# Performance work log

Measured on AMD Instinct MI355X. Metric: run time of the kernel, lower is better.

Reference implementation:

```python
import jax, jax.numpy as jnp
import numpy as np
import math

NUM_HEADS = 16
HIDDEN = 1024
MLP = 4096
SEQ = 2048
HEAD_DIM = HIDDEN // NUM_HEADS  # 64
EPS = 1e-5


def setup_inputs() -> dict:
    key = jax.random.key(0)
    ks = jax.random.split(key, 16)
    s = 0.02
    inp = {
        "x": jax.random.normal(ks[0], (SEQ, HIDDEN), jnp.float32),
        "rope_cos": jnp.cos(jnp.arange(SEQ, dtype=jnp.float32)[:, None] * (1.0 / (10000.0 ** (jnp.arange(HEAD_DIM // 2, dtype=jnp.float32) * 2 / HEAD_DIM)))[None, :]),
        "rope_sin": jnp.sin(jnp.arange(SEQ, dtype=jnp.float32)[:, None] * (1.0 / (10000.0 ** (jnp.arange(HEAD_DIM // 2, dtype=jnp.float32) * 2 / HEAD_DIM)))[None, :]),
        "norm0_w": jnp.ones((HIDDEN,), jnp.float32),
        "norm0_b": jnp.zeros((HIDDEN,), jnp.float32),
        "norm1_w": jnp.ones((HIDDEN,), jnp.float32),
        "norm1_b": jnp.zeros((HIDDEN,), jnp.float32),
        "wqkv_w": jax.random.normal(ks[1], (3 * HIDDEN, HIDDEN), jnp.float32) * s,
        "wqkv_b": jnp.zeros((3 * HIDDEN,), jnp.float32),
        "wo_w": jax.random.normal(ks[2], (HIDDEN, HIDDEN), jnp.float32) * s,
        "wo_b": jnp.zeros((HIDDEN,), jnp.float32),
        "up_w": jax.random.normal(ks[3], (MLP, HIDDEN), jnp.float32) * s,
        "up_b": jnp.zeros((MLP,), jnp.float32),
        "down_w": jax.random.normal(ks[4], (HIDDEN, MLP), jnp.float32) * s,
        "down_b": jnp.zeros((HIDDEN,), jnp.float32),
        # 4 packed sequences of length 512 each
        "input_row_offsets": jnp.array([0, 512, 1024, 1536, 2048], jnp.int32),
    }
    return inp


def _layernorm(x, w, b):
    m = jnp.mean(x, axis=-1, keepdims=True)
    v = jnp.mean((x - m) ** 2, axis=-1, keepdims=True)
    return (x - m) * jax.lax.rsqrt(v + EPS) * w + b


def _rope(t, cos, sin):
    # t: [S, nh, hd]; cos/sin: [S, hd/2] -> complex rotation of adjacent pairs
    S, nh, hd = t.shape
    t2 = t.reshape(S, nh, hd // 2, 2)
    re, im = t2[..., 0], t2[..., 1]
    c = cos[:, None, :]
    s = sin[:, None, :]
    out = jnp.stack([re * c - im * s, re * s + im * c], axis=-1)
    return out.reshape(S, nh, hd)


def _block(x, rope_cos, rope_sin, norm0_w, norm0_b, wqkv_w, wqkv_b, wo_w, wo_b,
           up_w, up_b, down_w, down_b, norm1_w, norm1_b, input_row_offsets):
    S, H = x.shape
    nh, hd = NUM_HEADS, HEAD_DIM
    h = _layernorm(x, norm0_w, norm0_b)
    qkv = (h @ wqkv_w.T + wqkv_b).reshape(S, 3, nh, hd)
    q, k, v = qkv[:, 0], qkv[:, 1], qkv[:, 2]
    q = _rope(q, rope_cos, rope_sin)
    k = _rope(k, rope_cos, rope_sin)
    # block-diagonal bool mask added as 0/1 float (matches torch `attn_weight += bool_mask`)
    seg = jnp.searchsorted(input_row_offsets, jnp.arange(S), side="right") - 1
    mask = (seg[:, None] == seg[None, :]).astype(jnp.float32)  # [S, S]
    scores = jnp.einsum("shd,thd->hst", q, k) / math.sqrt(hd) + mask[None]
    attn = jax.nn.softmax(scores.astype(jnp.float32), axis=-1).astype(q.dtype)
    out = jnp.einsum("hst,thd->shd", attn, v).reshape(S, H)
    x = x + (out @ wo_w.T + wo_b)
    h = _layernorm(x, norm1_w, norm1_b)
    h = jax.nn.gelu(h @ up_w.T + up_b, approximate=True)
    return x + (h @ down_w.T + down_b)


def reference(x, rope_cos, rope_sin, norm0_w, norm0_b, norm1_w, norm1_b,
              wqkv_w, wqkv_b, wo_w, wo_b, up_w, up_b, down_w, down_b,
              input_row_offsets):
    return _block(x, rope_cos, rope_sin, norm0_w, norm0_b, wqkv_w, wqkv_b,
                  wo_w, wo_b, up_w, up_b, down_w, down_b, norm1_w, norm1_b,
                  input_row_offsets)
```

## Files before the change

### kernel.cpp

```cpp
#include <hip/hip_runtime.h>
#include <hip/hip_bf16.h>
#include <math.h>

#define SEQ 2048
#define HID 1024
#define NH 16
#define HD 64

using f32x4  = __attribute__((ext_vector_type(4))) float;
using bf16x8 = __attribute__((ext_vector_type(8))) short;
using bf16x4 = __attribute__((ext_vector_type(4))) short;

union U8 { unsigned int u[4]; bf16x8 v; short s[8]; };
union U4 { unsigned int u[2]; bf16x4 v; short s[4]; };

#if __has_builtin(__builtin_amdgcn_mfma_f32_16x16x16bf16_1k)
#define MFMA16(a, b, c) __builtin_amdgcn_mfma_f32_16x16x16bf16_1k(a, b, c, 0, 0, 0)
#else
__device__ __forceinline__ f32x4 mfma16_asm(bf16x4 a, bf16x4 b, f32x4 c) {
  asm volatile("v_mfma_f32_16x16x16_bf16 %0, %1, %2, %0\n\ts_nop 7\n\ts_nop 7"
               : "+v"(c) : "v"(a), "v"(b));
  return c;
}
#define MFMA16(a, b, c) mfma16_asm(a, b, c)
#endif

__device__ __forceinline__ short f2bf(float f) {
  unsigned int x = __float_as_uint(f);
  unsigned int r = (x + 0x7fffu + ((x >> 16) & 1u)) >> 16;
  return (short)(r & 0xffffu);
}

__device__ __forceinline__ unsigned int pkbf(float a, float b) {
  return ((unsigned int)(unsigned short)f2bf(a)) |
         (((unsigned int)(unsigned short)f2bf(b)) << 16);
}

__device__ __forceinline__ float bf2f_lo(unsigned int u) {
  return __uint_as_float((u & 0xffffu) << 16);
}
__device__ __forceinline__ float bf2f_hi(unsigned int u) {
  return __uint_as_float(u & 0xffff0000u);
}

__device__ __forceinline__ float fast_exp2(float x) {
#if __has_builtin(__builtin_amdgcn_exp2f)
  return __builtin_amdgcn_exp2f(x);
#else
  return exp2f(x);
#endif
}

__device__ __forceinline__ float fast_rcp(float x) {
#if __has_builtin(__builtin_amdgcn_rcpf)
  return __builtin_amdgcn_rcpf(x);
#else
  return 1.0f / x;
#endif
}

__device__ __forceinline__ void async_cp16(const void* g, void* l) {
  __builtin_amdgcn_global_load_lds(
      (__attribute__((address_space(1))) void*)(g),
      (__attribute__((address_space(3))) void*)(l), 16, 0, 0);
}

__global__ void cvt_all_kernel(const float* __restrict__ a, const float* __restrict__ b,
                               const float* __restrict__ c, const float* __restrict__ d,
                               short* __restrict__ oa, short* __restrict__ ob,
                               short* __restrict__ oc, short* __restrict__ od) {
  int i = blockIdx.x * blockDim.x + threadIdx.x;
  const float* src; short* dst; int off;
  if (i < 786432)        { src = a; dst = oa; off = i; }
  else if (i < 1048576)  { src = b; dst = ob; off = i - 786432; }
  else if (i < 2097152)  { src = c; dst = oc; off = i - 1048576; }
  else                   { src = d; dst = od; off = i - 2097152; }
  float4 v = ((const float4*)src)[off];
  short4 o;
  o.x = f2bf(v.x); o.y = f2bf(v.y); o.z = f2bf(v.z); o.w = f2bf(v.w);
  ((short4*)dst)[off] = o;
}

__global__ __launch_bounds__(256) void ln_kernel(const float* __restrict__ x,
    const float* __restrict__ w, const float* __restrict__ b, short* __restrict__ out) {
  int row = blockIdx.x;
  int tid = threadIdx.x;
  float4 v = ((const float4*)(x + (size_t)row * HID))[tid];
  float s  = v.x + v.y + v.z + v.w;
  float s2 = v.x*v.x + v.y*v.y + v.z*v.z + v.w*v.w;
#pragma unroll
  for (int o = 32; o >= 1; o >>= 1) {
    s  += __shfl_xor(s,  o);
    s2 += __shfl_xor(s2, o);
  }
  __shared__ float red[8];
  int wv = tid >> 6;
  if ((tid & 63) == 0) { red[wv] = s; red[4 + wv] = s2; }
  __syncthreads();
  float ts  = red[0] + red[1] + red[2] + red[3];
  float ts2 = red[4] + red[5] + red[6] + red[7];
  float mean = ts * (1.0f / HID);
  float var  = ts2 * (1.0f / HID) - mean * mean;
  float rs = rsqrtf(var + 1e-5f);
  float4 wv4 = ((const float4*)w)[tid];
  float4 bv4 = ((const float4*)b)[tid];
  short4 o;
  o.x = f2bf((v.x - mean) * rs * wv4.x + bv4.x);
  o.y = f2bf((v.y - mean) * rs * wv4.y + bv4.y);
  o.z = f2bf((v.z - mean) * rs * wv4.z + bv4.z);
  o.w = f2bf((v.w - mean) * rs * wv4.w + bv4.w);
  ((short4*)(out + (size_t)row * HID))[tid] = o;
}

__global__ void rope_qk_kernel(const short* __restrict__ qkvb,
    const float* __restrict__ cosb, const float* __restrict__ sinb,
    short* __restrict__ Qh, short* __restrict__ Kh) {
  int tid = blockIdx.x * blockDim.x + threadIdx.x;
  int s   = tid >> 10;
  int r   = tid & 1023;
  int j   = r >> 9;
  int rem = r & 511;
  int h   = rem >> 5;
  int i   = rem & 31;
  int d   = i * 2;
  unsigned int u = *(const unsigned int*)(qkvb + (size_t)s * 3072 + j * 1024 + h * 64 + d);
  float a = bf2f_lo(u), b = bf2f_hi(u);
  float c  = cosb[s * 32 + i];
  float sn = sinb[s * 32 + i];
  float scale = (j == 0) ? 0.18033688011112043f : 1.0f;
  unsigned int o = pkbf(scale * (a * c - b * sn), scale * (a * sn + b * c));
  short* dst = (j == 0 ? Qh : Kh) + ((size_t)h * SEQ + s) * HD + d;
  *(unsigned int*)dst = o;
}

__global__ __launch_bounds__(256) void vtrans_kernel(const short* __restrict__ qkvb,
                                                     short* __restrict__ Vt) {
  __shared__ short tile[64 * 72];
  int s0   = blockIdx.x * 64;
  int head = blockIdx.y;
  int tid  = threadIdx.x;
#pragma unroll
  for (int p = 0; p < 2; p++) {
    int seg = p * 256 + tid;
    int row = seg >> 3;
    int c8  = seg & 7;
    bf16x8 v = *(const bf16x8*)(qkvb + (size_t)(s0 + row) * 3072 + 2048 + head * 64 + c8 * 8);
    *(bf16x8*)(tile + row * 72 + c8 * 8) = v;
  }
  __syncthreads();
#pragma unroll
  for (int p = 0; p < 2; p++) {
    int seg = p * 256 + tid;
    int d   = seg >> 3;
    int sc  = seg & 7;
    U8 o;
#pragma unroll
    for (int j = 0; j < 8; j++) o.s[j] = tile[(sc * 8 + j) * 72 + d];
    *(bf16x8*)(Vt + ((size_t)head * HD + d) * SEQ + s0 + sc * 8) = o.v;
  }
}

template <int EPI>
__global__ __launch_bounds__(256) void gemm_bt_kernel(
    const short* __restrict__ A, const short* __restrict__ B,
    const float* __restrict__ bias, const float* __restrict__ resid,
    void* __restrict__ outp, int M, int N, int Klen, int Kstride) {
  __shared__ __attribute__((aligned(16))) short Alds[128 * 32];
  __shared__ __attribute__((aligned(16))) short Blds[128 * 32];
  int tid = threadIdx.x;
  int w    = tid >> 6;
  int lane = tid & 63;
  int lcol  = lane & 15;
  int lhalf = lane >> 4;
  int m0 = blockIdx.y * 128;
  int n0 = blockIdx.x * 128;
  int z  = blockIdx.z;
  int wm = (w & 1) * 64;
  int wn = (w >> 1) * 64;

  const short* apt[2];
  const short* bpt[2];
#pragma unroll
  for (int p = 0; p < 2; p++) {
    int seg = p * 256 + tid;
    int row = seg >> 2;
    int c   = (seg & 3) ^ ((row >> 1) & 3);
    apt[p] = A + (size_t)z * Klen + (size_t)(m0 + row) * Kstride + c * 8;
    bpt[p] = B + (size_t)z * Klen + (size_t)(n0 + row) * Kstride + c * 8;
  }
  int sw = (lhalf ^ ((lcol >> 1) & 3)) * 8;

  f32x4 acc[4][4];
#pragma unroll
  for (int i = 0; i < 4; i++)
#pragma unroll
    for (int j = 0; j < 4; j++) acc[i][j] = (f32x4){0.f, 0.f, 0.f, 0.f};

  for (int k0 = 0; k0 < Klen; k0 += 32) {
#pragma unroll
    for (int p = 0; p < 2; p++) {
      async_cp16(apt[p], Alds + p * 2048 + w * 512);  apt[p] += 32;
      async_cp16(bpt[p], Blds + p * 2048 + w * 512);  bpt[p] += 32;
    }
    __syncthreads();
    bf16x8 af[4], bfr[4];
#pragma unroll
    for (int i = 0; i < 4; i++)
      af[i] = *(const bf16x8*)(Alds + (wm + i * 16 + lcol) * 32 + sw);
#pragma unroll
    for (int j = 0; j < 4; j++)
      bfr[j] = *(const bf16x8*)(Blds + (wn + j * 16 + lcol) * 32 + sw);
#pragma unroll
    for (int i = 0; i < 4; i++)
#pragma unroll
      for (int j = 0; j < 4; j++)
        acc[i][j] = __builtin_amdgcn_mfma_f32_16x16x32_bf16(af[i], bfr[j], acc[i][j], 0, 0, 0);
    __syncthreads();
  }

  float* outf = (float*)outp + (EPI == 4 ? (size_t)z * M * N : 0);
#pragma unroll
  for (int i = 0; i < 4; i++) {
#pragma unroll
    for (int j = 0; j < 4; j++) {
#pragma unroll
      for (int r = 0; r < 4; r++) {
        int row = m0 + wm + i * 16 + lhalf * 4 + r;
        int col = n0 + wn + j * 16 + lcol;
        float v = acc[i][j][r];
        if (EPI != 4) v += bias[col];
        if (EPI == 2) {
          float t = v * (1.5957691216057308f + 0.07135481283942279f * v * v);
          float e = fast_exp2(t * -1.4426950408889634f);
          v = v * fast_rcp(1.0f + e);
          ((short*)outp)[(size_t)row * N + col] = f2bf(v);
        } else if (EPI == 3) {
          ((short*)outp)[(size_t)row * N + col] = f2bf(v);
        } else {
          outf[(size_t)row * N + col] = v;
        }
      }
    }
  }
}

__global__ __launch_bounds__(256) void attn_kernel(
    const short* __restrict__ Qh, const short* __restrict__ Kh,
    const short* __restrict__ Vt, const int* __restrict__ offs,
    short* __restrict__ Opart, float* __restrict__ Lpart) {
  __shared__ __attribute__((aligned(16))) short Klds[64 * 64];
  __shared__ __attribute__((aligned(16))) short Vlds[64 * 64];
  int head = blockIdx.y;
  int q0   = blockIdx.x * 128;
  int z    = blockIdx.z;
  int tid  = threadIdx.x;
  int w    = tid >> 6;
  int lane = tid & 63;
  int lcol = lane & 15;
  int h    = lane >> 4;
  int s7   = lcol & 7;
  int o1 = offs[1], o2 = offs[2], o3 = offs[3];

  int qrowA = q0 + w * 16 + lcol;
  int qrowB = qrowA + 64;
  const short* qbA = Qh + ((size_t)head * SEQ + qrowA) * HD;
  const short* qbB = Qh + ((size_t)head * SEQ + qrowB) * HD;
  bf16x8 qf0a = *(const bf16x8*)(qbA + h * 8);
  bf16x8 qf1a = *(const bf16x8*)(qbA + 32 + h * 8);
  bf16x8 qf0b = *(const bf16x8*)(qbB + h * 8);
  bf16x8 qf1b = *(const bf16x8*)(qbB + 32 + h * 8);
  int sqA = (qrowA >= o1) + (qrowA >= o2) + (qrowA >= o3);
  int sqB = (qrowB >= o1) + (qrowB >= o2) + (qrowB >= o3);
  U8 qeA, qeB;
#pragma unroll
  for (int i = 0; i < 4; i++) { qeA.u[i] = 0; qeB.u[i] = 0; }
  if (h == 0) { qeA.s[sqA] = (short)0x3FB9; qeB.s[sqB] = (short)0x3FB9; }

  bf16x4 ones4;
#pragma unroll
  for (int i = 0; i < 4; i++) ones4[i] = (short)0x3F80;

  int kbase0 = lcol * 64 + ((h ^ s7) * 8);
  int kbase1 = lcol * 64 + (((4 + h) ^ s7) * 8);
  int vbase[4];
#pragma unroll
  for (int n = 0; n < 4; n++)
    vbase[n] = lcol * 64 + (((n * 2 + (h >> 1)) ^ s7) * 8) + (h & 1) * 4;

  int tbeg = z * 512;
  const short* kp0; const short* kp1; const short* vp0; const short* vp1;
  {
    int seg = tid, row = seg >> 3, g = (seg & 7) ^ (row & 7);
    kp0 = Kh + ((size_t)head * SEQ + tbeg + row) * HD + g * 8;
    vp0 = Vt + ((size_t)head * HD + row) * SEQ + tbeg + g * 8;
    seg = 256 + tid; row = seg >> 3; g = (seg & 7) ^ (row & 7);
    kp1 = Kh + ((size_t)head * SEQ + tbeg + row) * HD + g * 8;
    vp1 = Vt + ((size_t)head * HD + row) * SEQ + tbeg + g * 8;
  }

  f32x4 oA[4], oB[4];
#pragma unroll
  for (int nt = 0; nt < 4; nt++) {
    oA[nt] = (f32x4){0.f, 0.f, 0.f, 0.f};
    oB[nt] = (f32x4){0.f, 0.f, 0.f, 0.f};
  }
  f32x4 lA = (f32x4){0.f, 0.f, 0.f, 0.f};
  f32x4 lB = (f32x4){0.f, 0.f, 0.f, 0.f};

  for (int t0 = 0; t0 < 512; t0 += 64) {
    async_cp16(kp0, Klds + w * 512);          kp0 += 64 * HD;
    async_cp16(kp1, Klds + 2048 + w * 512);   kp1 += 64 * HD;
    async_cp16(vp0, Vlds + w * 512);          vp0 += 64;
    async_cp16(vp1, Vlds + 2048 + w * 512);   vp1 += 64;
    __syncthreads();

#pragma unroll
    for (int n = 0; n < 4; n++) {
      bf16x8 kf0 = *(const bf16x8*)(Klds + n * 1024 + kbase0);
      bf16x8 kf1 = *(const bf16x8*)(Klds + n * 1024 + kbase1);
      int key = tbeg + t0 + n * 16 + lcol;
      int sk = (key >= o1) + (key >= o2) + (key >= o3);
      U8 ke;
      ke.u[0] = (h == 0) ? ((sk == 0) ? 0x00003F80u : (sk == 1) ? 0x3F800000u : 0u) : 0u;
      ke.u[1] = (h == 0) ? ((sk == 2) ? 0x00003F80u : (sk == 3) ? 0x3F800000u : 0u) : 0u;
      ke.u[2] = 0; ke.u[3] = 0;

      f32x4 sA = (f32x4){0.f, 0.f, 0.f, 0.f};
      sA = __builtin_amdgcn_mfma_f32_16x16x32_bf16(kf0, qf0a, sA, 0, 0, 0);
      sA = __builtin_amdgcn_mfma_f32_16x16x32_bf16(kf1, qf1a, sA, 0, 0, 0);
      sA = __builtin_amdgcn_mfma_f32_16x16x32_bf16(ke.v, qeA.v, sA, 0, 0, 0);
      f32x4 sB = (f32x4){0.f, 0.f, 0.f, 0.f};
      sB = __builtin_amdgcn_mfma_f32_16x16x32_bf16(kf0, qf0b, sB, 0, 0, 0);
      sB = __builtin_amdgcn_mfma_f32_16x16x32_bf16(kf1, qf1b, sB, 0, 0, 0);
      sB = __builtin_amdgcn_mfma_f32_16x16x32_bf16(ke.v, qeB.v, sB, 0, 0, 0);

      float a0 = fast_exp2(sA[0]), a1 = fast_exp2(sA[1]);
      float a2 = fast_exp2(sA[2]), a3 = fast_exp2(sA[3]);
      float b0 = fast_exp2(sB[0]), b1 = fast_exp2(sB[1]);
      float b2 = fast_exp2(sB[2]), b3 = fast_exp2(sB[3]);
      U4 pA, pB;
      pA.u[0] = __builtin_amdgcn_perm(__float_as_uint(a1), __float_as_uint(a0), 0x07060302);
      pA.u[1] = __builtin_amdgcn_perm(__float_as_uint(a3), __float_as_uint(a2), 0x07060302);
      pB.u[0] = __builtin_amdgcn_perm(__float_as_uint(b1), __float_as_uint(b0), 0x07060302);
      pB.u[1] = __builtin_amdgcn_perm(__float_as_uint(b3), __float_as_uint(b2), 0x07060302);

#pragma unroll
      for (int nt = 0; nt < 4; nt++) {
        bf16x4 vf = *(const bf16x4*)(Vlds + nt * 1024 + vbase[n]);
        oA[nt] = MFMA16(vf, pA.v, oA[nt]);
        oB[nt] = MFMA16(vf, pB.v, oB[nt]);
      }
      lA = MFMA16(ones4, pA.v, lA);
      lB = MFMA16(ones4, pB.v, lB);
    }
    __syncthreads();
  }

  short* opA = Opart + ((size_t)z * SEQ + qrowA) * HID + head * HD + h * 4;
  short* opB = Opart + ((size_t)z * SEQ + qrowB) * HID + head * HD + h * 4;
#pragma unroll
  for (int nt = 0; nt < 4; nt++) {
    uint2 ua, ub;
    ua.x = pkbf(oA[nt][0], oA[nt][1]); ua.y = pkbf(oA[nt][2], oA[nt][3]);
    ub.x = pkbf(oB[nt][0], oB[nt][1]); ub.y = pkbf(oB[nt][2], oB[nt][3]);
    *(uint2*)(opA + nt * 16) = ua;
    *(uint2*)(opB + nt * 16) = ub;
  }
  if (lane < 16) {
    Lpart[((size_t)z * NH + head) * SEQ + qrowA] = lA[0];
    Lpart[((size_t)z * NH + head) * SEQ + qrowB] = lB[0];
  }
}

__global__ __launch_bounds__(256) void attn_merge_kernel(
    const short* __restrict__ Opart, const float* __restrict__ Lpart,
    short* __restrict__ attn) {
  int i = blockIdx.x * blockDim.x + threadIdx.x;
  int col4 = i & 255;
  int row  = i >> 8;
  int head = col4 >> 4;
  float acc0 = 0.f, acc1 = 0.f, acc2 = 0.f, acc3 = 0.f, l = 0.f;
#pragma unroll
  for (int zz = 0; zz < 4; zz++) {
    uint2 p = ((const uint2*)(Opart + (size_t)zz * SEQ * HID))[i];
    acc0 += bf2f_lo(p.x); acc1 += bf2f_hi(p.x);
    acc2 += bf2f_lo(p.y); acc3 += bf2f_hi(p.y);
    l += Lpart[((size_t)zz * NH + head) * SEQ + row];
  }
  float rl = fast_rcp(l);
  uint2 o;
  o.x = pkbf(acc0 * rl, acc1 * rl);
  o.y = pkbf(acc2 * rl, acc3 * rl);
  ((uint2*)attn)[i] = o;
}

__global__ __launch_bounds__(256) void merge_ln_kernel(
    const float* __restrict__ part, const float* __restrict__ bias,
    const float* __restrict__ resid, const float* __restrict__ w,
    const float* __restrict__ b, float* __restrict__ x1, short* __restrict__ h1) {
  int row = blockIdx.x;
  int tid = threadIdx.x;
  size_t idx = (size_t)row * HID / 4 + tid;
  float4 v = ((const float4*)part)[idx];
#pragma unroll
  for (int z = 1; z < 4; z++) {
    float4 q = ((const float4*)part)[(size_t)z * SEQ * HID / 4 + idx];
    v.x += q.x; v.y += q.y; v.z += q.z; v.w += q.w;
  }
  float4 bi = ((const float4*)bias)[tid];
  float4 rs4 = ((const float4*)(resid + (size_t)row * HID))[tid];
  v.x += bi.x + rs4.x; v.y += bi.y + rs4.y; v.z += bi.z + rs4.z; v.w += bi.w + rs4.w;
  ((float4*)(x1 + (size_t)row * HID))[tid] = v;
  float s  = v.x + v.y + v.z + v.w;
  float s2 = v.x*v.x + v.y*v.y + v.z*v.z + v.w*v.w;
#pragma unroll
  for (int o = 32; o >= 1; o >>= 1) {
    s  += __shfl_xor(s,  o);
    s2 += __shfl_xor(s2, o);
  }
  __shared__ float red[8];
  int wv = tid >> 6;
  if ((tid & 63) == 0) { red[wv] = s; red[4 + wv] = s2; }
  __syncthreads();
  float ts  = red[0] + red[1] + red[2] + red[3];
  float ts2 = red[4] + red[5] + red[6] + red[7];
  float mean = ts * (1.0f / HID);
  float var  = ts2 * (1.0f / HID) - mean * mean;
  float rsq = rsqrtf(var + 1e-5f);
  float4 wv4 = ((const float4*)w)[tid];
  float4 bv4 = ((const float4*)b)[tid];
  short4 o;
  o.x = f2bf((v.x - mean) * rsq * wv4.x + bv4.x);
  o.y = f2bf((v.y - mean) * rsq * wv4.y + bv4.y);
  o.z = f2bf((v.z - mean) * rsq * wv4.z + bv4.z);
  o.w = f2bf((v.w - mean) * rsq * wv4.w + bv4.w);
  ((short4*)(h1 + (size_t)row * HID))[tid] = o;
}

__global__ __launch_bounds__(256) void merge_bias_kernel(
    const float* __restrict__ part, const float* __restrict__ bias,
    const float* __restrict__ resid, float* __restrict__ out) {
  int i = blockIdx.x * blockDim.x + threadIdx.x;
  int col4 = i & 255;
  float4 v = ((const float4*)part)[i];
#pragma unroll
  for (int z = 1; z < 4; z++) {
    float4 q = ((const float4*)part)[(size_t)z * SEQ * HID / 4 + i];
    v.x += q.x; v.y += q.y; v.z += q.z; v.w += q.w;
  }
  float4 bi = ((const float4*)bias)[col4];
  float4 rs = ((const float4*)resid)[i];
  float4 o;
  o.x = v.x + bi.x + rs.x;
  o.y = v.y + bi.y + rs.y;
  o.z = v.z + bi.z + rs.z;
  o.w = v.w + bi.w + rs.w;
  ((float4*)out)[i] = o;
}

extern "C" void kernel_launch(void* const* d_in, const int* in_sizes, int n_in,
                              void* d_out, int out_size, void* d_ws, size_t ws_size,
                              hipStream_t stream) {
  const float* x      = (const float*)d_in[0];
  const float* ropec  = (const float*)d_in[1];
  const float* ropes  = (const float*)d_in[2];
  const float* n0w    = (const float*)d_in[3];
  const float* n0b    = (const float*)d_in[4];
  const float* n1w    = (const float*)d_in[5];
  const float* n1b    = (const float*)d_in[6];
  const float* wqkv_w = (const float*)d_in[7];
  const float* wqkv_b = (const float*)d_in[8];
  const float* wo_w   = (const float*)d_in[9];
  const float* wo_b   = (const float*)d_in[10];
  const float* up_w   = (const float*)d_in[11];
  const float* up_b   = (const float*)d_in[12];
  const float* down_w = (const float*)d_in[13];
  const float* down_b = (const float*)d_in[14];
  const int*   offs   = (const int*)d_in[15];
  float* out = (float*)d_out;

  char* base = (char*)d_ws;
  short* wqkv_bf = (short*)(base + 0);
  short* wo_bf   = (short*)(base + 6291456);
  short* up_bf   = (short*)(base + 8388608);
  short* down_bf = (short*)(base + 16777216);
  short* h0      = (short*)(base + 25165824);
  short* qkv_bf  = (short*)(base + 29360128);
  short* Qh      = (short*)(base + 41943040);
  short* Kh      = (short*)(base + 46137344);
  short* Vt      = (short*)(base + 50331648);
  short* Opart   = (short*)(base + 54525952);
  float* Lpart   = (float*)(base + 71303168);
  short* attn    = (short*)(base + 71827456);
  float* x1      = (float*)(base + 76021760);
  short* h1      = (short*)(base + 84410368);
  float* wopart  = (float*)(base + 25165824);
  short* u       = (short*)(base + 25165824);
  float* dnpart  = (float*)(base + 41943040);

  cvt_all_kernel<<<12288, 256, 0, stream>>>(wqkv_w, wo_w, up_w, down_w,
                                            wqkv_bf, wo_bf, up_bf, down_bf);
  ln_kernel<<<2048, 256, 0, stream>>>(x, n0w, n0b, h0);
  gemm_bt_kernel<3><<<dim3(24, 16), 256, 0, stream>>>(h0, wqkv_bf, wqkv_b, nullptr,
                                                      qkv_bf, 2048, 3072, 1024, 1024);
  rope_qk_kernel<<<8192, 256, 0, stream>>>(qkv_bf, ropec, ropes, Qh, Kh);
  vtrans_kernel<<<dim3(32, 16), 256, 0, stream>>>(qkv_bf, Vt);
  attn_kernel<<<dim3(16, 16, 4), 256, 0, stream>>>(Qh, Kh, Vt, offs, Opart, Lpart);
  attn_merge_kernel<<<2048, 256, 0, stream>>>(Opart, Lpart, attn);
  gemm_bt_kernel<4><<<dim3(8, 16, 4), 256, 0, stream>>>(attn, wo_bf, nullptr, nullptr,
                                                        wopart, 2048, 1024, 256, 1024);
  merge_ln_kernel<<<2048, 256, 0, stream>>>(wopart, wo_b, x, n1w, n1b, x1, h1);
  gemm_bt_kernel<2><<<dim3(32, 16), 256, 0, stream>>>(h1, up_bf, up_b, nullptr,
                                                      u, 2048, 4096, 1024, 1024);
  gemm_bt_kernel<4><<<dim3(8, 16, 4), 256, 0, stream>>>(u, down_bf, nullptr, nullptr,
                                                        dnpart, 2048, 1024, 1024, 4096);
  merge_bias_kernel<<<2048, 256, 0, stream>>>(dnpart, down_b, x1, out);
}
```

Before: 313.2 us.

## Store split-K partials as bf16 and use 16x16x32 MFMA for attention PV

The split-K GEMM partials for the output projection and down projection are now written as bf16 instead of fp32, and the merge kernels convert and sum them. This halves the partial-sum write and read traffic at some cost in accuracy. In attention, the bf16 probabilities are staged through a per-wave LDS buffer so the PV product and row-sum can use the wider 16x16x32 MFMA instead of 16x16x16. That halves the MFMA count but adds LDS stores and loads per tile.

```diff
diff --git a/kernel.cpp b/kernel.cpp
--- a/kernel.cpp
+++ b/kernel.cpp
@@ -9,21 +9,8 @@
 
 using f32x4  = __attribute__((ext_vector_type(4))) float;
 using bf16x8 = __attribute__((ext_vector_type(8))) short;
-using bf16x4 = __attribute__((ext_vector_type(4))) short;
 
 union U8 { unsigned int u[4]; bf16x8 v; short s[8]; };
-union U4 { unsigned int u[2]; bf16x4 v; short s[4]; };
-
-#if __has_builtin(__builtin_amdgcn_mfma_f32_16x16x16bf16_1k)
-#define MFMA16(a, b, c) __builtin_amdgcn_mfma_f32_16x16x16bf16_1k(a, b, c, 0, 0, 0)
-#else
-__device__ __forceinline__ f32x4 mfma16_asm(bf16x4 a, bf16x4 b, f32x4 c) {
-  asm volatile("v_mfma_f32_16x16x16_bf16 %0, %1, %2, %0\n\ts_nop 7\n\ts_nop 7"
-               : "+v"(c) : "v"(a), "v"(b));
-  return c;
-}
-#define MFMA16(a, b, c) mfma16_asm(a, b, c)
-#endif
 
 __device__ __forceinline__ short f2bf(float f) {
   unsigned int x = __float_as_uint(f);
@@ -218,7 +205,6 @@
     __syncthreads();
   }
 
-  float* outf = (float*)outp + (EPI == 4 ? (size_t)z * M * N : 0);
 #pragma unroll
   for (int i = 0; i < 4; i++) {
 #pragma unroll
@@ -228,7 +214,7 @@
         int row = m0 + wm + i * 16 + lhalf * 4 + r;
         int col = n0 + wn + j * 16 + lcol;
         float v = acc[i][j][r];
-        if (EPI != 4) v += bias[col];
+        if (EPI != 5) v += bias[col];
         if (EPI == 2) {
           float t = v * (1.5957691216057308f + 0.07135481283942279f * v * v);
           float e = fast_exp2(t * -1.4426950408889634f);
@@ -237,7 +223,7 @@
         } else if (EPI == 3) {
           ((short*)outp)[(size_t)row * N + col] = f2bf(v);
         } else {
-          outf[(size_t)row * N + col] = v;
+          ((short*)outp)[(size_t)z * M * N + (size_t)row * N + col] = f2bf(v);
         }
       }
     }
@@ -250,6 +236,7 @@
     short* __restrict__ Opart, float* __restrict__ Lpart) {
   __shared__ __attribute__((aligned(16))) short Klds[64 * 64];
   __shared__ __attribute__((aligned(16))) short Vlds[64 * 64];
+  __shared__ __attribute__((aligned(16))) unsigned int Plds[4][2][16 * 34];
   int head = blockIdx.y;
   int q0   = blockIdx.x * 128;
   int z    = blockIdx.z;
@@ -258,7 +245,6 @@
   int lane = tid & 63;
   int lcol = lane & 15;
   int h    = lane >> 4;
-  int s7   = lcol & 7;
   int o1 = offs[1], o2 = offs[2], o3 = offs[3];
 
   int qrowA = q0 + w * 16 + lcol;
@@ -276,16 +262,9 @@
   for (int i = 0; i < 4; i++) { qeA.u[i] = 0; qeB.u[i] = 0; }
   if (h == 0) { qeA.s[sqA] = (short)0x3FB9; qeB.s[sqB] = (short)0x3FB9; }
 
-  bf16x4 ones4;
-#pragma unroll
-  for (int i = 0; i < 4; i++) ones4[i] = (short)0x3F80;
-
-  int kbase0 = lcol * 64 + ((h ^ s7) * 8);
-  int kbase1 = lcol * 64 + (((4 + h) ^ s7) * 8);
-  int vbase[4];
-#pragma unroll
-  for (int n = 0; n < 4; n++)
-    vbase[n] = lcol * 64 + (((n * 2 + (h >> 1)) ^ s7) * 8) + (h & 1) * 4;
+  bf16x8 ones;
+#pragma unroll
+  for (int i = 0; i < 8; i++) ones[i] = 0x3F80;
 
   int tbeg = z * 512;
   const short* kp0; const short* kp1; const short* vp0; const short* vp1;
@@ -316,9 +295,12 @@
 
 #pragma unroll
     for (int n = 0; n < 4; n++) {
-      bf16x8 kf0 = *(const bf16x8*)(Klds + n * 1024 + kbase0);
-      bf16x8 kf1 = *(const bf16x8*)(Klds + n * 1024 + kbase1);
-      int key = tbeg + t0 + n * 16 + lcol;
+      int krow = n * 16 + lcol;
+      int r7 = krow & 7;
+      const short* ka = Klds + krow * 64;
+      bf16x8 kf0 = *(const bf16x8*)(ka + (h ^ r7) * 8);
+      bf16x8 kf1 = *(const bf16x8*)(ka + ((4 + h) ^ r7) * 8);
+      int key = tbeg + t0 + krow;
       int sk = (key >= o1) + (key >= o2) + (key >= o3);
       U8 ke;
       ke.u[0] = (h == 0) ? ((sk == 0) ? 0x00003F80u : (sk == 1) ? 0x3F800000u : 0u) : 0u;
@@ -338,20 +320,34 @@
       float a2 = fast_exp2(sA[2]), a3 = fast_exp2(sA[3]);
       float b0 = fast_exp2(sB[0]), b1 = fast_exp2(sB[1]);
       float b2 = fast_exp2(sB[2]), b3 = fast_exp2(sB[3]);
-      U4 pA, pB;
-      pA.u[0] = __builtin_amdgcn_perm(__float_as_uint(a1), __float_as_uint(a0), 0x07060302);
-      pA.u[1] = __builtin_amdgcn_perm(__float_as_uint(a3), __float_as_uint(a2), 0x07060302);
-      pB.u[0] = __builtin_amdgcn_perm(__float_as_uint(b1), __float_as_uint(b0), 0x07060302);
-      pB.u[1] = __builtin_amdgcn_perm(__float_as_uint(b3), __float_as_uint(b2), 0x07060302);
-
+      uint2 pwA, pwB;
+      pwA.x = __builtin_amdgcn_perm(__float_as_uint(a1), __float_as_uint(a0), 0x07060302);
+      pwA.y = __builtin_amdgcn_perm(__float_as_uint(a3), __float_as_uint(a2), 0x07060302);
+      pwB.x = __builtin_amdgcn_perm(__float_as_uint(b1), __float_as_uint(b0), 0x07060302);
+      pwB.y = __builtin_amdgcn_perm(__float_as_uint(b3), __float_as_uint(b2), 0x07060302);
+      *(uint2*)&Plds[w][0][lcol * 34 + n * 8 + h * 2] = pwA;
+      *(uint2*)&Plds[w][1][lcol * 34 + n * 8 + h * 2] = pwB;
+    }
+
+#pragma unroll
+    for (int kc = 0; kc < 2; kc++) {
+      int base = lcol * 34 + kc * 16 + h * 4;
+      uint2 a0 = *(const uint2*)&Plds[w][0][base];
+      uint2 a1 = *(const uint2*)&Plds[w][0][base + 2];
+      uint2 b0 = *(const uint2*)&Plds[w][1][base];
+      uint2 b1 = *(const uint2*)&Plds[w][1][base + 2];
+      U8 puA, puB;
+      puA.u[0] = a0.x; puA.u[1] = a0.y; puA.u[2] = a1.x; puA.u[3] = a1.y;
+      puB.u[0] = b0.x; puB.u[1] = b0.y; puB.u[2] = b1.x; puB.u[3] = b1.y;
 #pragma unroll
       for (int nt = 0; nt < 4; nt++) {
-        bf16x4 vf = *(const bf16x4*)(Vlds + nt * 1024 + vbase[n]);
-        oA[nt] = MFMA16(vf, pA.v, oA[nt]);
-        oB[nt] = MFMA16(vf, pB.v, oB[nt]);
+        int vrow = nt * 16 + lcol;
+        bf16x8 vf = *(const bf16x8*)(Vlds + vrow * 64 + (((kc * 4 + h) ^ (vrow & 7)) * 8));
+        oA[nt] = __builtin_amdgcn_mfma_f32_16x16x32_bf16(vf, puA.v, oA[nt], 0, 0, 0);
+        oB[nt] = __builtin_amdgcn_mfma_f32_16x16x32_bf16(vf, puB.v, oB[nt], 0, 0, 0);
       }
-      lA = MFMA16(ones4, pA.v, lA);
-      lB = MFMA16(ones4, pB.v, lB);
+      lA = __builtin_amdgcn_mfma_f32_16x16x32_bf16(ones, puA.v, lA, 0, 0, 0);
+      lB = __builtin_amdgcn_mfma_f32_16x16x32_bf16(ones, puB.v, lB, 0, 0, 0);
     }
     __syncthreads();
   }
@@ -395,17 +391,18 @@
 }
 
 __global__ __launch_bounds__(256) void merge_ln_kernel(
-    const float* __restrict__ part, const float* __restrict__ bias,
+    const short* __restrict__ part, const float* __restrict__ bias,
     const float* __restrict__ resid, const float* __restrict__ w,
     const float* __restrict__ b, float* __restrict__ x1, short* __restrict__ h1) {
   int row = blockIdx.x;
   int tid = threadIdx.x;
   size_t idx = (size_t)row * HID / 4 + tid;
-  float4 v = ((const float4*)part)[idx];
-#pragma unroll
-  for (int z = 1; z < 4; z++) {
-    float4 q = ((const float4*)part)[(size_t)z * SEQ * HID / 4 + idx];
-    v.x += q.x; v.y += q.y; v.z += q.z; v.w += q.w;
+  float4 v = {0.f, 0.f, 0.f, 0.f};
+#pragma unroll
+  for (int z = 0; z < 4; z++) {
+    uint2 p = ((const uint2*)(part + (size_t)z * SEQ * HID))[idx];
+    v.x += bf2f_lo(p.x); v.y += bf2f_hi(p.x);
+    v.z += bf2f_lo(p.y); v.w += bf2f_hi(p.y);
   }
   float4 bi = ((const float4*)bias)[tid];
   float4 rs4 = ((const float4*)(resid + (size_t)row * HID))[tid];
@@ -438,15 +435,16 @@
 }
 
 __global__ __launch_bounds__(256) void merge_bias_kernel(
-    const float* __restrict__ part, const float* __restrict__ bias,
+    const short* __restrict__ part, const float* __restrict__ bias,
     const float* __restrict__ resid, float* __restrict__ out) {
   int i = blockIdx.x * blockDim.x + threadIdx.x;
   int col4 = i & 255;
-  float4 v = ((const float4*)part)[i];
-#pragma unroll
-  for (int z = 1; z < 4; z++) {
-    float4 q = ((const float4*)part)[(size_t)z * SEQ * HID / 4 + i];
-    v.x += q.x; v.y += q.y; v.z += q.z; v.w += q.w;
+  float4 v = {0.f, 0.f, 0.f, 0.f};
+#pragma unroll
+  for (int z = 0; z < 4; z++) {
+    uint2 p = ((const uint2*)(part + (size_t)z * SEQ * HID))[i];
+    v.x += bf2f_lo(p.x); v.y += bf2f_hi(p.x);
+    v.z += bf2f_lo(p.y); v.w += bf2f_hi(p.y);
   }
   float4 bi = ((const float4*)bias)[col4];
   float4 rs = ((const float4*)resid)[i];
@@ -494,9 +492,9 @@
   short* attn    = (short*)(base + 71827456);
   float* x1      = (float*)(base + 76021760);
   short* h1      = (short*)(base + 84410368);
-  float* wopart  = (float*)(base + 25165824);
+  short* wopart  = (short*)(base + 25165824);
   short* u       = (short*)(base + 25165824);
-  float* dnpart  = (float*)(base + 41943040);
+  short* dnpart  = (short*)(base + 41943040);
 
   cvt_all_kernel<<<12288, 256, 0, stream>>>(wqkv_w, wo_w, up_w, down_w,
                                             wqkv_bf, wo_bf, up_bf, down_bf);
@@ -507,12 +505,12 @@
   vtrans_kernel<<<dim3(32, 16), 256, 0, stream>>>(qkv_bf, Vt);
   attn_kernel<<<dim3(16, 16, 4), 256, 0, stream>>>(Qh, Kh, Vt, offs, Opart, Lpart);
   attn_merge_kernel<<<2048, 256, 0, stream>>>(Opart, Lpart, attn);
-  gemm_bt_kernel<4><<<dim3(8, 16, 4), 256, 0, stream>>>(attn, wo_bf, nullptr, nullptr,
+  gemm_bt_kernel<5><<<dim3(8, 16, 4), 256, 0, stream>>>(attn, wo_bf, nullptr, nullptr,
                                                         wopart, 2048, 1024, 256, 1024);
   merge_ln_kernel<<<2048, 256, 0, stream>>>(wopart, wo_b, x, n1w, n1b, x1, h1);
   gemm_bt_kernel<2><<<dim3(32, 16), 256, 0, stream>>>(h1, up_bf, up_b, nullptr,
                                                       u, 2048, 4096, 1024, 1024);
-  gemm_bt_kernel<4><<<dim3(8, 16, 4), 256, 0, stream>>>(u, down_bf, nullptr, nullptr,
+  gemm_bt_kernel<5><<<dim3(8, 16, 4), 256, 0, stream>>>(u, down_bf, nullptr, nullptr,
                                                         dnpart, 2048, 1024, 1024, 4096);
   merge_bias_kernel<<<2048, 256, 0, stream>>>(dnpart, down_b, x1, out);
 }
```

Result: no change. 316.2 us (+1.0%).
